# Kernel optimization log

Measured on AMD Instinct MI355X. Metric: run time of the kernel, lower is better.

The kernel has to match this reference:

```python
import jax, jax.numpy as jnp
import numpy as np

N_NODES = 150000  # num_users + num_items
EMB_DIM = 64
N_EDGES = 4000000


def setup_inputs() -> dict:
    key = jax.random.key(0)
    k1, k2 = jax.random.split(key)
    x = jax.random.normal(k1, (N_NODES, EMB_DIM), dtype=jnp.float32)
    edge_index = jax.random.randint(k2, (2, N_EDGES), 0, N_NODES, dtype=jnp.int64)
    return {"x": x, "edge_index": edge_index}


def _lgconv(x, row, col, w):
    # message: x[row] * w ; aggregate: scatter-add into col
    msg = x[row] * w[:, None]  # [E, D]
    return jax.ops.segment_sum(msg, col, num_segments=N_NODES)


def reference(x, edge_index):
    row, col = edge_index[0], edge_index[1]
    # gcn_norm without self-loops: deg from target index (col)
    deg = jax.ops.segment_sum(jnp.ones(row.shape[0], x.dtype), col,
                              num_segments=N_NODES)
    dis = jnp.where(deg > 0, jax.lax.rsqrt(jnp.maximum(deg, 1.0)), 0.0)
    w = dis[row] * dis[col]  # [E]

    emb0 = x
    emb1 = _lgconv(emb0, row, col, w)
    emb2 = _lgconv(emb1, row, col, w)
    # stack over layer dim then mean == mean of the three layer embeddings
    out = (emb0 + emb1 + emb2) / 3.0
    return out
```

## Files before the change

kernel.cpp:

```cpp
#include <hip/hip_runtime.h>
#include <hip/hip_bf16.h>


#define EMB_DIM 64
#define BUCKET_BITS 9
#define BUCKET_SZ 512
#define EPB 8192
#define NBMAX 512
#define CAP 16384
#define GSTRIDE 16

typedef float f32x4 __attribute__((ext_vector_type(4)));

__device__ __forceinline__ float bf_lo(unsigned int q) { return __uint_as_float(q << 16); }
__device__ __forceinline__ float bf_hi(unsigned int q) { return __uint_as_float(q & 0xffff0000u); }
__device__ __forceinline__ unsigned int f2bf(float f) {
    unsigned int u = __float_as_uint(f);
    return (u + 0x7fffu + ((u >> 16) & 1u)) >> 16;
}

__global__ void init_kernel(int* __restrict__ gcur, int* __restrict__ offsets,
                            int NB, int N, int E) {
    int t = threadIdx.x;
    if (t < NB) gcur[t * GSTRIDE] = t * CAP;
    if (t == 0) offsets[N] = E;
}

__global__ void fused_scatter(const int* __restrict__ rows,
                              const int* __restrict__ cols,
                              int* __restrict__ gcur,
                              unsigned int* __restrict__ pairs,
                              int E, int NB) {
    __shared__ unsigned int sbuf[EPB];
    __shared__ unsigned short sbkt[EPB];
    __shared__ int lh[NBMAX];
    __shared__ int lexc[NBMAX];
    __shared__ int ldiff[NBMAX];
    __shared__ int lrank[NBMAX];
    __shared__ int wsum[8];
    int blk = blockIdx.x, t = threadIdx.x;
    for (int b = t; b < NBMAX; b += 1024) lh[b] = 0;
    __syncthreads();
    int start = blk * EPB, end = min(start + EPB, E);
    int nloc = end - start;
    int myc[8], myr[8];
#pragma unroll
    for (int j = 0; j < 8; ++j) {
        int i = start + t + j * 1024;
        if (i < end) {
            myc[j] = cols[i];
            myr[j] = rows[i];
            atomicAdd(&lh[myc[j] >> BUCKET_BITS], 1);
        } else {
            myc[j] = -1;
        }
    }
    __syncthreads();
    int v = 0, incl = 0;
    if (t < 512) {
        v = lh[t];
        incl = v;
        int lane = t & 63;
#pragma unroll
        for (int off = 1; off < 64; off <<= 1) {
            int u = __shfl_up(incl, off, 64);
            if (lane >= off) incl += u;
        }
        if (lane == 63) wsum[t >> 6] = incl;
    }
    __syncthreads();
    if (t < 8) {
        int s = wsum[t];
        int inc2 = s;
#pragma unroll
        for (int off = 1; off < 8; off <<= 1) {
            int u = __shfl_up(inc2, off, 64);
            if (t >= off) inc2 += u;
        }
        wsum[t] = inc2 - s;
    }
    __syncthreads();
    int myexc = 0;
    if (t < 512) {
        myexc = (incl - v) + wsum[t >> 6];
        lexc[t] = myexc;
    }
    if (t < NB) {
        int c = lh[t];
        int gb = c ? atomicAdd(&gcur[t * GSTRIDE], c) : 0;
        ldiff[t] = gb - myexc;
        lrank[t] = 0;
    }
    __syncthreads();
#pragma unroll
    for (int j = 0; j < 8; ++j) {
        if (myc[j] >= 0) {
            int b = myc[j] >> BUCKET_BITS;
            int rk = atomicAdd(&lrank[b], 1);
            int p = lexc[b] + rk;
            sbuf[p] = (unsigned)myr[j] |
                      ((unsigned)(myc[j] & (BUCKET_SZ - 1)) << 18);
            sbkt[p] = (unsigned short)b;
        }
    }
    __syncthreads();
    for (int p = t; p < nloc; p += 1024) {
        int b = sbkt[p];
        pairs[ldiff[b] + p] = sbuf[p];
    }
}

__global__ void bucket_finalize(const unsigned int* __restrict__ pairs,
                                const int* __restrict__ gcur,
                                int* __restrict__ edata,
                                int* __restrict__ offsets,
                                float* __restrict__ dis,
                                int N, int E, int NB) {
    __shared__ int sbuf[CAP];
    __shared__ int ccnt[BUCKET_SZ];
    __shared__ int cexc[BUCKET_SZ];
    __shared__ int rnk[BUCKET_SZ];
    __shared__ int wsum[16];
    __shared__ int gb_s;
    int b = blockIdx.x, t = threadIdx.x;
    int pbase = b * CAP;
    int cnt = gcur[b * GSTRIDE] - pbase;

    int part = 0;
    for (int j = t; j < b; j += 1024) part += gcur[j * GSTRIDE] - j * CAP;
#pragma unroll
    for (int off = 32; off; off >>= 1) part += __shfl_down(part, off, 64);
    if ((t & 63) == 0) wsum[t >> 6] = part;
    if (t < BUCKET_SZ) ccnt[t] = 0;
    __syncthreads();
    if (t == 0) {
        int g = 0;
#pragma unroll
        for (int w = 0; w < 16; ++w) g += wsum[w];
        gb_s = g;
    }
    for (int i = t; i < cnt; i += 1024)
        atomicAdd(&ccnt[pairs[pbase + i] >> 18], 1);
    __syncthreads();

    int v = 0, incl = 0;
    if (t < 512) {
        v = ccnt[t];
        incl = v;
        int lane = t & 63;
#pragma unroll
        for (int off = 1; off < 64; off <<= 1) {
            int u = __shfl_up(incl, off, 64);
            if (lane >= off) incl += u;
        }
        if (lane == 63) wsum[t >> 6] = incl;
    }
    __syncthreads();
    if (t < 8) {
        int s = wsum[t];
        int inc2 = s;
#pragma unroll
        for (int off = 1; off < 8; off <<= 1) {
            int u = __shfl_up(inc2, off, 64);
            if (t >= off) inc2 += u;
        }
        wsum[t] = inc2 - s;
    }
    __syncthreads();
    if (t < 512) cexc[t] = (incl - v) + wsum[t >> 6];
    if (t < BUCKET_SZ) rnk[t] = 0;
    __syncthreads();

    int base = gb_s;
    int col0 = b << BUCKET_BITS;
    int ncols = min(BUCKET_SZ, N - col0);
    if (t < ncols) {
        int c = ccnt[t];
        offsets[col0 + t] = base + cexc[t];
        dis[col0 + t] = (c > 0) ? rsqrtf((float)c) : 0.0f;
    }
    __syncthreads();
    for (int i = t; i < cnt; i += 1024) {
        unsigned p = pairs[pbase + i];
        int lc = p >> 18;
        int rk = atomicAdd(&rnk[lc], 1);
        sbuf[cexc[lc] + rk] = p & 0x3FFFF;
    }
    __syncthreads();
    for (int i = t; i < cnt; i += 1024)
        edata[base + i] = sbuf[i];
}

__global__ void yb_kernel(const float* __restrict__ x,
                          const float* __restrict__ dis,
                          unsigned short* __restrict__ yb, int N) {
    int tid = blockIdx.x * blockDim.x + threadIdx.x;
    int nth = gridDim.x * blockDim.x;
    int total = N * 16;
    for (int u = tid; u < total; u += nth) {
        int lr = u >> 4;
        int part = u & 15;
        float d = dis[lr];
        size_t o = (((size_t)lr) << 6) + part * 4;
        float4 vx = *(const float4*)(x + o);
        uint2 w;
        w.x = f2bf(vx.x * d) | (f2bf(vx.y * d) << 16);
        w.y = f2bf(vx.z * d) | (f2bf(vx.w * d) << 16);
        *(uint2*)(yb + o) = w;
    }
}

__device__ __forceinline__ void acc8(float* acc, uint4 q) {
    acc[0] += bf_lo(q.x);
    acc[1] += bf_hi(q.x);
    acc[2] += bf_lo(q.y);
    acc[3] += bf_hi(q.y);
    acc[4] += bf_lo(q.z);
    acc[5] += bf_hi(q.z);
    acc[6] += bf_lo(q.w);
    acc[7] += bf_hi(q.w);
}

template <bool FINAL>
__global__ void agg_kernel(const unsigned short* __restrict__ embb,
                           const int* __restrict__ edata,
                           const int* __restrict__ offsets,
                           const float* __restrict__ dis,
                           const float* __restrict__ x,
                           unsigned short* __restrict__ outb,
                           float* __restrict__ outf,
                           int n) {
    int wave = (blockIdx.x * blockDim.x + threadIdx.x) >> 6;
    int lane = threadIdx.x & 63;
    int sub = lane >> 3;
    int dest = (wave << 3) + sub;
    if (dest >= n) return;
    int dimo = (lane & 7) * 8;

    int s = offsets[dest];
    int e = offsets[dest + 1];

    float a0[8] = {0, 0, 0, 0, 0, 0, 0, 0};
    float a1[8] = {0, 0, 0, 0, 0, 0, 0, 0};
    const unsigned short* eb = embb + dimo;

    int k = s;
    int kfull = s + ((e - s) & ~7);
    for (; k < kfull; k += 8) {
        int s0 = edata[k];
        int s1 = edata[k + 1];
        int s2 = edata[k + 2];
        int s3 = edata[k + 3];
        int s4 = edata[k + 4];
        int s5 = edata[k + 5];
        int s6 = edata[k + 6];
        int s7 = edata[k + 7];
        uint4 q0 = *(const uint4*)(eb + ((size_t)s0 << 6));
        uint4 q1 = *(const uint4*)(eb + ((size_t)s1 << 6));
        uint4 q2 = *(const uint4*)(eb + ((size_t)s2 << 6));
        uint4 q3 = *(const uint4*)(eb + ((size_t)s3 << 6));
        uint4 q4 = *(const uint4*)(eb + ((size_t)s4 << 6));
        uint4 q5 = *(const uint4*)(eb + ((size_t)s5 << 6));
        uint4 q6 = *(const uint4*)(eb + ((size_t)s6 << 6));
        uint4 q7 = *(const uint4*)(eb + ((size_t)s7 << 6));
        acc8(a0, q0);
        acc8(a1, q1);
        acc8(a0, q2);
        acc8(a1, q3);
        acc8(a0, q4);
        acc8(a1, q5);
        acc8(a0, q6);
        acc8(a1, q7);
    }
    if (k < e) {
        int s0 = edata[k];
        int s1 = (k + 1 < e) ? edata[k + 1] : -1;
        int s2 = (k + 2 < e) ? edata[k + 2] : -1;
        int s3 = (k + 3 < e) ? edata[k + 3] : -1;
        int s4 = (k + 4 < e) ? edata[k + 4] : -1;
        int s5 = (k + 5 < e) ? edata[k + 5] : -1;
        int s6 = (k + 6 < e) ? edata[k + 6] : -1;
        int s7 = (k + 7 < e) ? edata[k + 7] : -1;
        uint4 q0, q1, q2, q3, q4, q5, q6, q7;
        q0 = *(const uint4*)(eb + ((size_t)s0 << 6));
        if (s1 >= 0) q1 = *(const uint4*)(eb + ((size_t)s1 << 6));
        if (s2 >= 0) q2 = *(const uint4*)(eb + ((size_t)s2 << 6));
        if (s3 >= 0) q3 = *(const uint4*)(eb + ((size_t)s3 << 6));
        if (s4 >= 0) q4 = *(const uint4*)(eb + ((size_t)s4 << 6));
        if (s5 >= 0) q5 = *(const uint4*)(eb + ((size_t)s5 << 6));
        if (s6 >= 0) q6 = *(const uint4*)(eb + ((size_t)s6 << 6));
        if (s7 >= 0) q7 = *(const uint4*)(eb + ((size_t)s7 << 6));
        acc8(a0, q0);
        if (s1 >= 0) acc8(a1, q1);
        if (s2 >= 0) acc8(a0, q2);
        if (s3 >= 0) acc8(a1, q3);
        if (s4 >= 0) acc8(a0, q4);
        if (s5 >= 0) acc8(a1, q5);
        if (s6 >= 0) acc8(a0, q6);
        if (s7 >= 0) acc8(a1, q7);
    }

    float acc[8];
#pragma unroll
    for (int j = 0; j < 8; ++j) acc[j] = a0[j] + a1[j];

    float dc = dis[dest];
    size_t o = ((size_t)dest << 6) + dimo;
    if (FINAL) {
        float rd = (dc > 0.0f) ? 1.0f / dc : 0.0f;
        f32x4 xa = __builtin_nontemporal_load((const f32x4*)(x + o));
        f32x4 xc = __builtin_nontemporal_load((const f32x4*)(x + o) + 1);
        uint4 qz = *(const uint4*)(embb + o);
        const float k3 = 1.0f / 3.0f;
        f32x4 r0, r1;
        r0.x = (xa.x + bf_lo(qz.x) * rd + dc * acc[0]) * k3;
        r0.y = (xa.y + bf_hi(qz.x) * rd + dc * acc[1]) * k3;
        r0.z = (xa.z + bf_lo(qz.y) * rd + dc * acc[2]) * k3;
        r0.w = (xa.w + bf_hi(qz.y) * rd + dc * acc[3]) * k3;
        r1.x = (xc.x + bf_lo(qz.z) * rd + dc * acc[4]) * k3;
        r1.y = (xc.y + bf_hi(qz.z) * rd + dc * acc[5]) * k3;
        r1.z = (xc.z + bf_lo(qz.w) * rd + dc * acc[6]) * k3;
        r1.w = (xc.w + bf_hi(qz.w) * rd + dc * acc[7]) * k3;
        __builtin_nontemporal_store(r0, (f32x4*)(outf + o));
        __builtin_nontemporal_store(r1, (f32x4*)(outf + o) + 1);
    } else {
        float zs = dc * dc;
        uint4 q;
        q.x = f2bf(zs * acc[0]) | (f2bf(zs * acc[1]) << 16);
        q.y = f2bf(zs * acc[2]) | (f2bf(zs * acc[3]) << 16);
        q.z = f2bf(zs * acc[4]) | (f2bf(zs * acc[5]) << 16);
        q.w = f2bf(zs * acc[6]) | (f2bf(zs * acc[7]) << 16);
        *(uint4*)(outb + o) = q;
    }
}

extern "C" void kernel_launch(void* const* d_in, const int* in_sizes, int n_in,
                              void* d_out, int out_size, void* d_ws, size_t ws_size,
                              hipStream_t stream) {
    const float* x  = (const float*)d_in[0];
    const int*   ei = (const int*)d_in[1];
    const int E = in_sizes[1] / 2;
    const int N = in_sizes[0] / EMB_DIM;

    const int* rows = ei;
    const int* cols = ei + E;

    const int NB = (N + BUCKET_SZ - 1) >> BUCKET_BITS;
    const int NBLK = (E + EPB - 1) / EPB;

    int*   gcur    = (int*)d_ws;
    float* dis     = (float*)(gcur + 512 * GSTRIDE);
    int*   offsets = (int*)(dis + 150080);
    int*   edata   = offsets + 150080;
    unsigned short* yb = (unsigned short*)(edata + E);
    unsigned short* zb = yb + (size_t)N * EMB_DIM;
    unsigned int* pairs = (unsigned int*)zb;
    float* out = (float*)d_out;

    init_kernel<<<1, 512, 0, stream>>>(gcur, offsets, NB, N, E);
    fused_scatter<<<NBLK, 1024, 0, stream>>>(rows, cols, gcur, pairs, E, NB);
    bucket_finalize<<<NB, 1024, 0, stream>>>(pairs, gcur, edata, offsets,
                                             dis, N, E, NB);
    yb_kernel<<<2048, 256, 0, stream>>>(x, dis, yb, N);

    int agg_waves = (N + 7) / 8;
    int agg_blocks = (agg_waves + 3) / 4;
    agg_kernel<false><<<agg_blocks, 256, 0, stream>>>(yb, edata, offsets, dis,
                                                      nullptr, zb, nullptr, N);
    agg_kernel<true><<<agg_blocks, 256, 0, stream>>>(zb, edata, offsets, dis,
                                                     x, nullptr, out, N);
}
```

Before: 281.5 us.

## Split bucket finalize into half-bucket blocks and replace init kernel with memset

Each 512-column bucket is now finalized by two 512-thread blocks, each owning 256 columns, instead of one 1024-thread block. This doubles the block count (about 293 to 586) for better CU occupancy and halves shared-memory staging per block. The cost is that each block scans the full bucket's pairs twice and discards half. The init kernel is replaced by a memset of the counters, with bucket bases computed as t*CAP+old, and offsets[N] is now written inside yb_kernel.

```diff
diff --git a/kernel.cpp b/kernel.cpp
--- a/kernel.cpp
+++ b/kernel.cpp
@@ -8,6 +8,7 @@
 #define EPB 8192
 #define NBMAX 512
 #define CAP 16384
+#define HCAP 8192
 #define GSTRIDE 16
 
 typedef float f32x4 __attribute__((ext_vector_type(4)));
@@ -17,13 +18,6 @@
 __device__ __forceinline__ unsigned int f2bf(float f) {
     unsigned int u = __float_as_uint(f);
     return (u + 0x7fffu + ((u >> 16) & 1u)) >> 16;
-}
-
-__global__ void init_kernel(int* __restrict__ gcur, int* __restrict__ offsets,
-                            int NB, int N, int E) {
-    int t = threadIdx.x;
-    if (t < NB) gcur[t * GSTRIDE] = t * CAP;
-    if (t == 0) offsets[N] = E;
 }
 
 __global__ void fused_scatter(const int* __restrict__ rows,
@@ -87,8 +81,8 @@
     }
     if (t < NB) {
         int c = lh[t];
-        int gb = c ? atomicAdd(&gcur[t * GSTRIDE], c) : 0;
-        ldiff[t] = gb - myexc;
+        int old = c ? atomicAdd(&gcur[t * GSTRIDE], c) : 0;
+        ldiff[t] = (t * CAP + old) - myexc;
         lrank[t] = 0;
     }
     __syncthreads();
@@ -110,41 +104,45 @@
     }
 }
 
-__global__ void bucket_finalize(const unsigned int* __restrict__ pairs,
-                                const int* __restrict__ gcur,
-                                int* __restrict__ edata,
-                                int* __restrict__ offsets,
-                                float* __restrict__ dis,
-                                int N, int E, int NB) {
-    __shared__ int sbuf[CAP];
-    __shared__ int ccnt[BUCKET_SZ];
-    __shared__ int cexc[BUCKET_SZ];
-    __shared__ int rnk[BUCKET_SZ];
-    __shared__ int wsum[16];
-    __shared__ int gb_s;
-    int b = blockIdx.x, t = threadIdx.x;
+__global__ __launch_bounds__(512)
+void bucket_finalize(const unsigned int* __restrict__ pairs,
+                     const int* __restrict__ gcur,
+                     int* __restrict__ edata,
+                     int* __restrict__ offsets,
+                     float* __restrict__ dis,
+                     int N, int E, int NB) {
+    __shared__ int sbuf[HCAP];
+    __shared__ int ccnt[256];
+    __shared__ int cexc[256];
+    __shared__ int cur[256];
+    __shared__ int wsum[12];
+    __shared__ int gb_s, tot_s;
+    int bh = blockIdx.x, t = threadIdx.x;
+    int b = bh >> 1, h = bh & 1;
     int pbase = b * CAP;
-    int cnt = gcur[b * GSTRIDE] - pbase;
+    int cnt = gcur[b * GSTRIDE];
 
     int part = 0;
-    for (int j = t; j < b; j += 1024) part += gcur[j * GSTRIDE] - j * CAP;
+    for (int j = t; j < b; j += 512) part += gcur[j * GSTRIDE];
 #pragma unroll
     for (int off = 32; off; off >>= 1) part += __shfl_down(part, off, 64);
     if ((t & 63) == 0) wsum[t >> 6] = part;
-    if (t < BUCKET_SZ) ccnt[t] = 0;
+    if (t < 256) ccnt[t] = 0;
     __syncthreads();
     if (t == 0) {
         int g = 0;
 #pragma unroll
-        for (int w = 0; w < 16; ++w) g += wsum[w];
+        for (int w = 0; w < 8; ++w) g += wsum[w];
         gb_s = g;
     }
-    for (int i = t; i < cnt; i += 1024)
-        atomicAdd(&ccnt[pairs[pbase + i] >> 18], 1);
+    for (int i = t; i < cnt; i += 512) {
+        int lc = (int)(pairs[pbase + i] >> 18);
+        if ((lc >> 8) == h) atomicAdd(&ccnt[lc & 255], 1);
+    }
     __syncthreads();
 
     int v = 0, incl = 0;
-    if (t < 512) {
+    if (t < 256) {
         v = ccnt[t];
         incl = v;
         int lane = t & 63;
@@ -156,45 +154,52 @@
         if (lane == 63) wsum[t >> 6] = incl;
     }
     __syncthreads();
-    if (t < 8) {
-        int s = wsum[t];
-        int inc2 = s;
-#pragma unroll
-        for (int off = 1; off < 8; off <<= 1) {
-            int u = __shfl_up(inc2, off, 64);
-            if (t >= off) inc2 += u;
-        }
-        wsum[t] = inc2 - s;
-    }
-    __syncthreads();
-    if (t < 512) cexc[t] = (incl - v) + wsum[t >> 6];
-    if (t < BUCKET_SZ) rnk[t] = 0;
-    __syncthreads();
-
-    int base = gb_s;
-    int col0 = b << BUCKET_BITS;
-    int ncols = min(BUCKET_SZ, N - col0);
-    if (t < ncols) {
+    if (t == 0) {
+        int tot = 0;
+#pragma unroll
+        for (int w = 0; w < 4; ++w) {
+            int s = wsum[w];
+            wsum[8 + w] = tot;
+            tot += s;
+        }
+        tot_s = tot;
+    }
+    __syncthreads();
+    if (t < 256) {
+        int e = (incl - v) + wsum[8 + (t >> 6)];
+        cexc[t] = e;
+        cur[t] = e;
+    }
+    __syncthreads();
+
+    int own = tot_s;
+    int base = gb_s + (h ? (cnt - own) : 0);
+    int col0 = (b << BUCKET_BITS) + (h << 8);
+    if (t < 256 && col0 + t < N) {
         int c = ccnt[t];
         offsets[col0 + t] = base + cexc[t];
         dis[col0 + t] = (c > 0) ? rsqrtf((float)c) : 0.0f;
     }
     __syncthreads();
-    for (int i = t; i < cnt; i += 1024) {
+    for (int i = t; i < cnt; i += 512) {
         unsigned p = pairs[pbase + i];
-        int lc = p >> 18;
-        int rk = atomicAdd(&rnk[lc], 1);
-        sbuf[cexc[lc] + rk] = p & 0x3FFFF;
-    }
-    __syncthreads();
-    for (int i = t; i < cnt; i += 1024)
+        int lc = (int)(p >> 18);
+        if ((lc >> 8) == h) {
+            int rk = atomicAdd(&cur[lc & 255], 1);
+            sbuf[rk] = p & 0x3FFFF;
+        }
+    }
+    __syncthreads();
+    for (int i = t; i < own; i += 512)
         edata[base + i] = sbuf[i];
 }
 
 __global__ void yb_kernel(const float* __restrict__ x,
                           const float* __restrict__ dis,
-                          unsigned short* __restrict__ yb, int N) {
+                          unsigned short* __restrict__ yb,
+                          int* __restrict__ offsets, int N, int E) {
     int tid = blockIdx.x * blockDim.x + threadIdx.x;
+    if (tid == 0) offsets[N] = E;
     int nth = gridDim.x * blockDim.x;
     int total = N * 16;
     for (int u = tid; u < total; u += nth) {
@@ -357,11 +362,11 @@
     unsigned int* pairs = (unsigned int*)zb;
     float* out = (float*)d_out;
 
-    init_kernel<<<1, 512, 0, stream>>>(gcur, offsets, NB, N, E);
+    hipMemsetAsync(gcur, 0, 512 * GSTRIDE * sizeof(int), stream);
     fused_scatter<<<NBLK, 1024, 0, stream>>>(rows, cols, gcur, pairs, E, NB);
-    bucket_finalize<<<NB, 1024, 0, stream>>>(pairs, gcur, edata, offsets,
-                                             dis, N, E, NB);
-    yb_kernel<<<2048, 256, 0, stream>>>(x, dis, yb, N);
+    bucket_finalize<<<NB * 2, 512, 0, stream>>>(pairs, gcur, edata, offsets,
+                                                dis, N, E, NB);
+    yb_kernel<<<2048, 256, 0, stream>>>(x, dis, yb, offsets, N, E);
 
     int agg_waves = (N + 7) / 8;
     int agg_blocks = (agg_waves + 3) / 4;
```

After: 290.2 us. 3.1% more time.
